# Performance work log

Hardware: AMD Instinct MI355X
Metric: run time of the kernel (lower is better)

The kernel has to match this reference:

```python
import jax, jax.numpy as jnp
import numpy as np

S, B, D, W = 2048, 4, 1024, 256  # seq_len, batch, d_model, local_window_size


def create_local_mask(seq_len, w):
    # Faithful to source: tril(w-1) then tril(-(w-1)) -> keeps j <= i-(w-1)
    m = jnp.ones((seq_len, seq_len), dtype=bool)
    m = jnp.tril(m, w - 1)
    m = jnp.tril(m, -(w - 1))
    return m


def setup_inputs() -> dict:
    key = jax.random.key(0)
    ks = jax.random.split(key, 12)
    w = lambda k: jax.random.normal(k, (D, D), dtype=jnp.float32) * 0.02
    return {
        "query": jax.random.normal(ks[0], (S, B, D), dtype=jnp.float32),
        "key_in": jax.random.normal(ks[1], (S, B, D), dtype=jnp.float32),
        "value": jax.random.normal(ks[2], (S, B, D), dtype=jnp.float32),
        "Wq": w(ks[3]), "bq": jnp.zeros((D,), jnp.float32),
        "Wk": w(ks[4]), "bk": jnp.zeros((D,), jnp.float32),
        "Wv": w(ks[5]), "bv": jnp.zeros((D,), jnp.float32),
        "pos_bias": jax.random.normal(ks[6], (S, S), dtype=jnp.float32) * 0.02,
        "Wo": w(ks[7]), "bo": jnp.zeros((D,), jnp.float32),
        "mask": jnp.ones((S, S, 1), dtype=bool),
    }


def reference(query, key_in, value, Wq, bq, Wk, bk, Wv, bv, pos_bias, Wo, bo, mask):
    # Linear projections (torch Linear: x @ W.T + b)
    q = jnp.einsum('sbd,ed->sbe', query, Wq) + bq
    k = jnp.einsum('sbd,ed->sbe', key_in, Wk) + bk
    v = jnp.einsum('sbd,ed->sbe', value, Wv) + bv

    local_mask = create_local_mask(S, W)
    pb = (pos_bias * local_mask.astype(pos_bias.dtype))[:, :, None]  # [S,S,1]
    pb = jnp.where(mask, pb, -jnp.inf)

    max_key = jnp.max(k, axis=0, keepdims=True)          # [1,B,D]
    max_pb = jnp.max(pb, axis=1, keepdims=True)          # [S,1,1]
    exp_key = jnp.exp(k - max_key)                       # [S,B,D]
    exp_pb = jnp.exp(pb - max_pb)                        # [S,S,B] after broadcast

    num = jnp.einsum('ijb,jbd->ibd', exp_pb, exp_key * v)
    den = jnp.einsum('ijb,jbd->ibd', exp_pb, exp_key)
    y = jax.nn.sigmoid(q) * num / den
    return jnp.einsum('sbd,ed->sbe', y, Wo) + bo
```

## Files before the change

kernel.cpp:

```cpp
#include <hip/hip_runtime.h>
#include <hip/hip_bf16.h>
#include <cstdint>


typedef short short8 __attribute__((ext_vector_type(8)));
typedef float f32x4 __attribute__((ext_vector_type(4)));

#define S_LEN 2048
#define NBD 4096
#define SBD 8388608
#define DD 1048576
#define SS 4194304

#define ASZ 8192
#define BUFSZ 24576
#define AS1 __attribute__((address_space(1)))
#define AS3 __attribute__((address_space(3)))

__device__ __forceinline__ unsigned short f2bf(float f) {
  union { float f; unsigned int u; } x; x.f = f;
  unsigned int u = x.u;
  unsigned int r = u + 0x7fffu + ((u >> 16) & 1u);
  return (unsigned short)(r >> 16);
}
__device__ __forceinline__ float bf2f(unsigned short b) {
  union { unsigned int u; float f; } x; x.u = ((unsigned int)b) << 16;
  return x.f;
}

__global__ void k_cvt3(const float* __restrict__ a, const float* __restrict__ b,
                       const float* __restrict__ c, unsigned short* __restrict__ oa,
                       unsigned short* __restrict__ ob, unsigned short* __restrict__ oc) {
  int i = (blockIdx.x * blockDim.x + threadIdx.x) * 4;
  float4 fa = *(const float4*)(a + i);
  float4 fb = *(const float4*)(b + i);
  float4 fc = *(const float4*)(c + i);
  ushort4 ua, ub, uc;
  ua.x = f2bf(fa.x); ua.y = f2bf(fa.y); ua.z = f2bf(fa.z); ua.w = f2bf(fa.w);
  ub.x = f2bf(fb.x); ub.y = f2bf(fb.y); ub.z = f2bf(fb.z); ub.w = f2bf(fb.w);
  uc.x = f2bf(fc.x); uc.y = f2bf(fc.y); uc.z = f2bf(fc.z); uc.w = f2bf(fc.w);
  *(ushort4*)(oa + i) = ua;
  *(ushort4*)(ob + i) = ub;
  *(ushort4*)(oc + i) = uc;
}

__global__ void k_cvt4w(const float* __restrict__ wq, const float* __restrict__ wk,
                        const float* __restrict__ wv, const float* __restrict__ wo,
                        unsigned short* __restrict__ wcat, unsigned short* __restrict__ wob) {
  int i = (blockIdx.x * blockDim.x + threadIdx.x) * 4;
  float4 fq = *(const float4*)(wq + i);
  float4 fk = *(const float4*)(wk + i);
  float4 fv = *(const float4*)(wv + i);
  float4 fo = *(const float4*)(wo + i);
  ushort4 u;
  u.x = f2bf(fq.x); u.y = f2bf(fq.y); u.z = f2bf(fq.z); u.w = f2bf(fq.w);
  *(ushort4*)(wcat + i) = u;
  u.x = f2bf(fk.x); u.y = f2bf(fk.y); u.z = f2bf(fk.z); u.w = f2bf(fk.w);
  *(ushort4*)(wcat + DD + i) = u;
  u.x = f2bf(fv.x); u.y = f2bf(fv.y); u.z = f2bf(fv.z); u.w = f2bf(fv.w);
  *(ushort4*)(wcat + 2 * DD + i) = u;
  u.x = f2bf(fo.x); u.y = f2bf(fo.y); u.z = f2bf(fo.z); u.w = f2bf(fo.w);
  *(ushort4*)(wob + i) = u;
}

__global__ void k_build_c(const float* __restrict__ pb, unsigned short* __restrict__ C) {
  int idx = blockIdx.x * blockDim.x + threadIdx.x;
  int i = idx >> 11;
  int j = idx & 2047;
  float v = (i >= j + 255) ? expm1f(pb[idx]) : 0.0f;
  C[idx] = f2bf(v);
}

__global__ __launch_bounds__(256) void k_eu_transpose(
    const unsigned short* __restrict__ kbf, const unsigned short* __restrict__ vbf,
    unsigned short* __restrict__ Mt, float* __restrict__ totals) {
  __shared__ unsigned short Lu[64][65];
  __shared__ unsigned short Le[64][65];
  const int n0 = blockIdx.x * 64;
  const int j0 = blockIdx.y * 64;
  const int t = threadIdx.x;
  const int c = t & 63;
  const int jq = t >> 6;
  float ptu = 0.f, pte = 0.f;
#pragma unroll 4
  for (int s = 0; s < 16; ++s) {
    int jj = jq + s * 4;
    size_t g = (size_t)(j0 + jj) * NBD + n0 + c;
    float kv = bf2f(kbf[g]);
    float vv = bf2f(vbf[g]);
    float e = __expf(kv);
    float u = e * vv;
    Le[jj][c] = f2bf(e);
    Lu[jj][c] = f2bf(u);
    pte += e; ptu += u;
  }
  atomicAdd(&totals[n0 + c], ptu);
  atomicAdd(&totals[NBD + n0 + c], pte);
  __syncthreads();
  const int jj2 = t & 63;
  const int nq = t >> 6;
#pragma unroll 4
  for (int s = 0; s < 16; ++s) {
    int nn = nq + s * 4;
    int ru = 2 * n0 + 32 * (nn >> 4) + (nn & 15);
    Mt[(size_t)ru * S_LEN + j0 + jj2] = Lu[jj2][nn];
    Mt[(size_t)(ru + 16) * S_LEN + j0 + jj2] = Le[jj2][nn];
  }
}


#define SBAR() do { __builtin_amdgcn_sched_barrier(0); __builtin_amdgcn_s_barrier(); \
                    __builtin_amdgcn_sched_barrier(0); } while (0)
#define VM(n)  do { asm volatile("s_waitcnt vmcnt(" #n ")" ::: "memory"); \
                    __builtin_amdgcn_sched_barrier(0); } while (0)
#define LGK0() do { asm volatile("s_waitcnt lgkmcnt(0)" ::: "memory"); \
                    __builtin_amdgcn_sched_barrier(0); } while (0)

#define STAGE(tile, bidx) do {                                                            \
    const int k0s_ = (tile) * 64;                                                         \
    _Pragma("unroll") for (int q_ = 0; q_ < 2; ++q_) {                                    \
      const int g_ = wave * 2 + q_;                                                       \
      __builtin_amdgcn_global_load_lds(                                                   \
          (const AS1 unsigned int*)(Ag + (size_t)(m0 + g_ * 8 + lr) * LDA + k0s_ + lc),   \
          (AS3 unsigned int*)&lds[(bidx) * BUFSZ + g_ * 512], 16, 0, 0);                  \
    }                                                                                     \
    _Pragma("unroll") for (int q_ = 0; q_ < 4; ++q_) {                                    \
      const int g_ = wave * 4 + q_;                                                       \
      __builtin_amdgcn_global_load_lds(                                                   \
          (const AS1 unsigned int*)(Bg + (size_t)(n0 + g_ * 8 + lr) * LDB + k0s_ + lc),   \
          (AS3 unsigned int*)&lds[(bidx) * BUFSZ + ASZ + g_ * 512], 16, 0, 0);            \
    }                                                                                     \
  } while (0)

#define READF(RA, RB, bidx, ks) do {                                                      \
    const int kof_ = (ks) * 32 + lh8;                                                     \
    _Pragma("unroll") for (int f_ = 0; f_ < 4; ++f_) {                                    \
      const int row_ = wr + f_ * 16 + l15;                                                \
      RA[f_] = *(const short8*)&lds[(bidx) * BUFSZ + row_ * 64 + (kof_ ^ swz)];           \
    }                                                                                     \
    _Pragma("unroll") for (int f_ = 0; f_ < 4; ++f_) {                                    \
      const int row_ = wc + f_ * 16 + l15;                                                \
      RB[f_] = *(const short8*)&lds[(bidx) * BUFSZ + ASZ + row_ * 64 + (kof_ ^ swz)];     \
    }                                                                                     \
  } while (0)

#define MFMA16(RA, RB) do {                                                               \
    __builtin_amdgcn_s_setprio(1);                                                        \
    _Pragma("unroll") for (int i_ = 0; i_ < 4; ++i_)                                      \
    _Pragma("unroll") for (int j_ = 0; j_ < 4; ++j_)                                      \
      acc[i_][j_] = __builtin_amdgcn_mfma_f32_16x16x32_bf16(RA[i_], RB[j_],               \
                                                            acc[i_][j_], 0, 0, 0);       \
    __builtin_amdgcn_s_setprio(0);                                                        \
  } while (0)

template <int MODE>
__global__ __launch_bounds__(512, 2) void k_gemm8(
    const unsigned short* __restrict__ A0, const unsigned short* __restrict__ A1,
    const unsigned short* __restrict__ A2, const unsigned short* __restrict__ Bg,
    const float* __restrict__ x0, const float* __restrict__ x1, const float* __restrict__ x2,
    const unsigned short* __restrict__ sq,
    void* __restrict__ out0, void* __restrict__ out1, void* __restrict__ out2) {
  __shared__ unsigned short lds[3 * BUFSZ];

  const int tid = threadIdx.x;
  const int wave = tid >> 6, lane = tid & 63;
  const int l15 = lane & 15, lh = lane >> 4;
  const int lh8 = lh * 8;
  const int swz = (l15 & 7) * 8;
  const int lr = lane >> 3;
  const int lc = ((lane & 7) ^ lr) * 8;
  const int wr = (wave >> 2) * 64, wc = (wave & 3) * 64;

  const int w = blockIdx.x;
  int mb, nb;
  if (MODE == 0) { const int xcd = w & 7, slot = w >> 3; mb = xcd * 8 + slot / 12; nb = slot % 12; }
  else if (MODE == 1) { mb = 15 - (w >> 5); nb = w & 31; }
  else { const int xcd = w & 7, slot = w >> 3; mb = xcd * 8 + (slot >> 2); nb = slot & 3; }
  const int m0 = mb * 128, n0 = nb * 256;
  const int LDA = (MODE == 1) ? 2048 : 1024;
  const int LDB = (MODE == 1) ? 2048 : 1024;
  const int NT = (MODE == 1) ? (mb > 0 ? 2 * mb - 1 : 0) : 16;
  const int grp = (MODE == 0) ? (nb >> 2) : 0;
  const unsigned short* Ag = (MODE == 0) ? (grp == 0 ? A0 : (grp == 1 ? A1 : A2)) : A0;

  f32x4 acc[4][4];
#pragma unroll
  for (int i = 0; i < 4; ++i)
#pragma unroll
    for (int j = 0; j < 4; ++j)
      acc[i][j] = (f32x4){0.f, 0.f, 0.f, 0.f};

  short8 ra0[4], rb0[4], ra1[4], rb1[4];

  if (NT > 0) {
    STAGE(0, 0);
    if (NT > 1) STAGE(1, 1);
    if (NT > 2) STAGE(2, 2);
    if (NT > 2) VM(12); else if (NT > 1) VM(6); else VM(0);
    SBAR();
    READF(ra0, rb0, 0, 0);
    int cb = 0;
    for (int t = 0; t < NT; ++t) {
      READF(ra1, rb1, cb, 1);
      MFMA16(ra0, rb0);
      if (t < NT - 1) {
        LGK0();
        if (t + 2 <= NT - 1) VM(6); else VM(0);
        SBAR();
        int nbuf = cb + 1; if (nbuf == 3) nbuf = 0;
        READF(ra0, rb0, nbuf, 0);
        if (t + 3 <= NT - 1) STAGE(t + 3, cb);
        cb = nbuf;
        MFMA16(ra1, rb1);
      } else {
        MFMA16(ra1, rb1);
      }
    }
  }

  if (MODE == 0) {
    const float* bias = grp == 0 ? x0 : (grp == 1 ? x1 : x2);
    unsigned short* outp = (unsigned short*)(grp == 0 ? out0 : (grp == 1 ? out1 : out2));
#pragma unroll
    for (int i = 0; i < 4; ++i)
#pragma unroll
      for (int j = 0; j < 4; ++j)
#pragma unroll
        for (int r = 0; r < 4; ++r) {
          const int row = m0 + wr + i * 16 + lh * 4 + r;
          const int col = (n0 + wc + j * 16 + l15) & 1023;
          float v = acc[i][j][r] + bias[col];
          if (grp == 0) v = 1.0f / (1.0f + __expf(-v));
          outp[(size_t)row * 1024 + col] = f2bf(v);
        }
  } else if (MODE == 1) {
    unsigned short* Y = (unsigned short*)out0;
#pragma unroll
    for (int i = 0; i < 4; ++i)
#pragma unroll
      for (int p = 0; p < 2; ++p) {
        const int n = ((n0 + wc) >> 1) + 16 * p + l15;
        const float tu = x0[n];
        const float te = x0[NBD + n];
#pragma unroll
        for (int r = 0; r < 4; ++r) {
          const int row = m0 + wr + i * 16 + lh * 4 + r;
          const size_t idx = (size_t)row * NBD + n;
          const float num = tu + acc[i][2 * p][r];
          const float den = te + acc[i][2 * p + 1][r];
          Y[idx] = f2bf(bf2f(sq[idx]) * num / den);
        }
      }
  } else {
    float* outp = (float*)out0;
#pragma unroll
    for (int i = 0; i < 4; ++i)
#pragma unroll
      for (int j = 0; j < 4; ++j)
#pragma unroll
        for (int r = 0; r < 4; ++r) {
          const int row = m0 + wr + i * 16 + lh * 4 + r;
          const int col = n0 + wc + j * 16 + l15;
          outp[(size_t)row * 1024 + col] = acc[i][j][r] + x0[col];
        }
  }
}

extern "C" void kernel_launch(void* const* d_in, const int* in_sizes, int n_in,
                              void* d_out, int out_size, void* d_ws, size_t ws_size,
                              hipStream_t stream) {
  const float* query   = (const float*)d_in[0];
  const float* key_in  = (const float*)d_in[1];
  const float* value   = (const float*)d_in[2];
  const float* Wq      = (const float*)d_in[3];
  const float* bq      = (const float*)d_in[4];
  const float* Wk      = (const float*)d_in[5];
  const float* bk      = (const float*)d_in[6];
  const float* Wv      = (const float*)d_in[7];
  const float* bv      = (const float*)d_in[8];
  const float* pos_bias= (const float*)d_in[9];
  const float* Wo      = (const float*)d_in[10];
  const float* bo      = (const float*)d_in[11];
  float* out = (float*)d_out;

  char* wp = (char*)d_ws;
  auto alloc = [&](size_t bytes) -> char* {
    char* p = wp;
    wp += (bytes + 255) & ~(size_t)255;
    return p;
  };
  unsigned short* Xq   = (unsigned short*)alloc((size_t)SBD * 2);
  unsigned short* Xk   = (unsigned short*)alloc((size_t)SBD * 2);
  unsigned short* Xv   = (unsigned short*)alloc((size_t)SBD * 2);
  unsigned short* Wcat = (unsigned short*)alloc((size_t)3 * DD * 2);
  unsigned short* Wob  = (unsigned short*)alloc((size_t)DD * 2);
  unsigned short* Cb   = (unsigned short*)alloc((size_t)SS * 2);
  unsigned short* sigq = (unsigned short*)alloc((size_t)SBD * 2);
  unsigned short* kbf  = (unsigned short*)alloc((size_t)SBD * 2);
  unsigned short* vbf  = (unsigned short*)alloc((size_t)SBD * 2);
  unsigned short* Mt   = (unsigned short*)alloc((size_t)8192 * S_LEN * 2);
  float*          tot  = (float*)alloc((size_t)8192 * 4);
  unsigned short* Yb   = (unsigned short*)alloc((size_t)SBD * 2);

  k_cvt3<<<SBD / 4 / 256, 256, 0, stream>>>(query, key_in, value, Xq, Xk, Xv);
  k_cvt4w<<<DD / 4 / 256, 256, 0, stream>>>(Wq, Wk, Wv, Wo, Wcat, Wob);

  k_build_c<<<SS / 256, 256, 0, stream>>>(pos_bias, Cb);

  k_gemm8<0><<<768, 512, 0, stream>>>(Xq, Xk, Xv, Wcat, bq, bk, bv, nullptr,
                                      sigq, kbf, vbf);

  hipMemsetAsync(tot, 0, 8192 * sizeof(float), stream);
  dim3 ge(NBD / 64, S_LEN / 64);
  k_eu_transpose<<<ge, 256, 0, stream>>>(kbf, vbf, Mt, tot);

  k_gemm8<1><<<512, 512, 0, stream>>>(Cb, nullptr, nullptr, Mt, tot, nullptr, nullptr,
                                      sigq, Yb, nullptr, nullptr);

  k_gemm8<2><<<256, 512, 0, stream>>>(Yb, nullptr, nullptr, Wob, bo, nullptr, nullptr,
                                      nullptr, out, nullptr, nullptr);
}
```

Before: 179.6 us.

## Fuse fp32-to-bf16 input conversion into the QKV projection GEMM

Removes the separate conversion kernel for query/key/value and its bf16 staging buffers. A new QKV GEMM kernel loads fp32 activations into registers, converts them to bf16, and writes them to LDS inside the pipelined main loop, while weights still stream through global_load_lds. This cuts a full read-and-write pass over three 32 MB inputs and one kernel launch. In exchange the GEMM reads twice the bytes for A and spends extra VALU work and register pressure on conversion inside the loop.

```diff
diff --git a/kernel.cpp b/kernel.cpp
--- a/kernel.cpp
+++ b/kernel.cpp
@@ -26,22 +26,6 @@
 __device__ __forceinline__ float bf2f(unsigned short b) {
   union { unsigned int u; float f; } x; x.u = ((unsigned int)b) << 16;
   return x.f;
-}
-
-__global__ void k_cvt3(const float* __restrict__ a, const float* __restrict__ b,
-                       const float* __restrict__ c, unsigned short* __restrict__ oa,
-                       unsigned short* __restrict__ ob, unsigned short* __restrict__ oc) {
-  int i = (blockIdx.x * blockDim.x + threadIdx.x) * 4;
-  float4 fa = *(const float4*)(a + i);
-  float4 fb = *(const float4*)(b + i);
-  float4 fc = *(const float4*)(c + i);
-  ushort4 ua, ub, uc;
-  ua.x = f2bf(fa.x); ua.y = f2bf(fa.y); ua.z = f2bf(fa.z); ua.w = f2bf(fa.w);
-  ub.x = f2bf(fb.x); ub.y = f2bf(fb.y); ub.z = f2bf(fb.z); ub.w = f2bf(fb.w);
-  uc.x = f2bf(fc.x); uc.y = f2bf(fc.y); uc.z = f2bf(fc.z); uc.w = f2bf(fc.w);
-  *(ushort4*)(oa + i) = ua;
-  *(ushort4*)(ob + i) = ub;
-  *(ushort4*)(oc + i) = uc;
 }
 
 __global__ void k_cvt4w(const float* __restrict__ wq, const float* __restrict__ wk,
@@ -108,13 +92,154 @@
   }
 }
 
-
 #define SBAR() do { __builtin_amdgcn_sched_barrier(0); __builtin_amdgcn_s_barrier(); \
                     __builtin_amdgcn_sched_barrier(0); } while (0)
 #define VM(n)  do { asm volatile("s_waitcnt vmcnt(" #n ")" ::: "memory"); \
                     __builtin_amdgcn_sched_barrier(0); } while (0)
 #define LGK0() do { asm volatile("s_waitcnt lgkmcnt(0)" ::: "memory"); \
                     __builtin_amdgcn_sched_barrier(0); } while (0)
+
+#define MFMA16(RA, RB) do {                                                               \
+    __builtin_amdgcn_s_setprio(1);                                                        \
+    _Pragma("unroll") for (int i_ = 0; i_ < 4; ++i_)                                      \
+    _Pragma("unroll") for (int j_ = 0; j_ < 4; ++j_)                                      \
+      acc[i_][j_] = __builtin_amdgcn_mfma_f32_16x16x32_bf16(RA[i_], RB[j_],               \
+                                                            acc[i_][j_], 0, 0, 0);       \
+    __builtin_amdgcn_s_setprio(0);                                                        \
+  } while (0)
+
+#define READF(RA, RB, bidx, ks) do {                                                      \
+    const int kof_ = (ks) * 32 + lh8;                                                     \
+    _Pragma("unroll") for (int f_ = 0; f_ < 4; ++f_) {                                    \
+      const int row_ = wr + f_ * 16 + l15;                                                \
+      RA[f_] = *(const short8*)&lds[(bidx) * BUFSZ + row_ * 64 + (kof_ ^ swz)];           \
+    }                                                                                     \
+    _Pragma("unroll") for (int f_ = 0; f_ < 4; ++f_) {                                    \
+      const int row_ = wc + f_ * 16 + l15;                                                \
+      RB[f_] = *(const short8*)&lds[(bidx) * BUFSZ + ASZ + row_ * 64 + (kof_ ^ swz)];     \
+    }                                                                                     \
+  } while (0)
+
+#define ALD(tile) do {                                                                    \
+    const float* p0_ = aP0 + (tile) * 64;                                                 \
+    const float* p1_ = aP1 + (tile) * 64;                                                 \
+    af00 = *(const float4*)p0_;  af01 = *(const float4*)(p0_ + 4);                        \
+    af10 = *(const float4*)p1_;  af11 = *(const float4*)(p1_ + 4);                        \
+  } while (0)
+
+#define ACVT(bidx) do {                                                                   \
+    short8 s0_, s1_;                                                                      \
+    s0_[0] = (short)f2bf(af00.x); s0_[1] = (short)f2bf(af00.y);                           \
+    s0_[2] = (short)f2bf(af00.z); s0_[3] = (short)f2bf(af00.w);                           \
+    s0_[4] = (short)f2bf(af01.x); s0_[5] = (short)f2bf(af01.y);                           \
+    s0_[6] = (short)f2bf(af01.z); s0_[7] = (short)f2bf(af01.w);                           \
+    s1_[0] = (short)f2bf(af10.x); s1_[1] = (short)f2bf(af10.y);                           \
+    s1_[2] = (short)f2bf(af10.z); s1_[3] = (short)f2bf(af10.w);                           \
+    s1_[4] = (short)f2bf(af11.x); s1_[5] = (short)f2bf(af11.y);                           \
+    s1_[6] = (short)f2bf(af11.z); s1_[7] = (short)f2bf(af11.w);                           \
+    *(short8*)&lds[(bidx) * BUFSZ + da0] = s0_;                                           \
+    *(short8*)&lds[(bidx) * BUFSZ + da1] = s1_;                                           \
+  } while (0)
+
+#define BSTG(tile, bidx) do {                                                             \
+    const int k0s_ = (tile) * 64;                                                         \
+    _Pragma("unroll") for (int q_ = 0; q_ < 4; ++q_) {                                    \
+      const int g_ = wave * 4 + q_;                                                       \
+      __builtin_amdgcn_global_load_lds(                                                   \
+          (const AS1 unsigned int*)(Bg + (size_t)(n0 + g_ * 8 + lr) * 1024 + k0s_ + lc),  \
+          (AS3 unsigned int*)&lds[(bidx) * BUFSZ + ASZ + g_ * 512], 16, 0, 0);            \
+    }                                                                                     \
+  } while (0)
+
+__global__ __launch_bounds__(512, 2) void k_qkvf32(
+    const float* __restrict__ A0, const float* __restrict__ A1,
+    const float* __restrict__ A2, const unsigned short* __restrict__ Bg,
+    const float* __restrict__ b0, const float* __restrict__ b1, const float* __restrict__ b2,
+    unsigned short* __restrict__ o0, unsigned short* __restrict__ o1,
+    unsigned short* __restrict__ o2) {
+  __shared__ unsigned short lds[3 * BUFSZ];
+
+  const int tid = threadIdx.x;
+  const int wave = tid >> 6, lane = tid & 63;
+  const int l15 = lane & 15, lh = lane >> 4;
+  const int lh8 = lh * 8;
+  const int swz = (l15 & 7) * 8;
+  const int lr = lane >> 3;
+  const int lq = lane & 7;
+  const int lc = (lq ^ lr) * 8;
+  const int wr = (wave >> 2) * 64, wc = (wave & 3) * 64;
+
+  const int w = blockIdx.x;
+  const int xcd = w & 7, slot = w >> 3;
+  const int mb = xcd * 8 + slot / 12;
+  const int nb = slot % 12;
+  const int m0 = mb * 128, n0 = nb * 256;
+  const int grp = nb >> 2;
+  const float* Af = grp == 0 ? A0 : (grp == 1 ? A1 : A2);
+
+  const float* aP0 = Af + (size_t)(m0 + (wave * 2 + 0) * 8 + lr) * 1024 + lc;
+  const float* aP1 = Af + (size_t)(m0 + (wave * 2 + 1) * 8 + lr) * 1024 + lc;
+  const int da0 = (wave * 2 + 0) * 512 + lane * 8;
+  const int da1 = (wave * 2 + 1) * 512 + lane * 8;
+
+  f32x4 acc[4][4];
+#pragma unroll
+  for (int i = 0; i < 4; ++i)
+#pragma unroll
+    for (int j = 0; j < 4; ++j)
+      acc[i][j] = (f32x4){0.f, 0.f, 0.f, 0.f};
+
+  float4 af00, af01, af10, af11;
+  short8 ra0[4], rb0[4], ra1[4], rb1[4];
+  const int NT = 16;
+
+  ALD(0); VM(0); ACVT(0);
+  ALD(1); BSTG(0, 0);
+  VM(4);  ACVT(1);
+  ALD(2); BSTG(1, 1);
+  VM(4);  ACVT(2);
+  ALD(3); BSTG(2, 2);
+  LGK0();
+  VM(8);
+  SBAR();
+  READF(ra0, rb0, 0, 0);
+  int cb = 0;
+  for (int t = 0; t < NT; ++t) {
+    READF(ra1, rb1, cb, 1);
+    MFMA16(ra0, rb0);
+    if (t < NT - 1) {
+      LGK0();
+      if (t <= NT - 3) VM(4); else VM(0);
+      SBAR();
+      int nbuf = cb + 1; if (nbuf == 3) nbuf = 0;
+      READF(ra0, rb0, nbuf, 0);
+      if (t + 3 <= NT - 1) ACVT(cb);
+      if (t + 4 <= NT - 1) ALD(t + 4);
+      if (t + 3 <= NT - 1) BSTG(t + 3, cb);
+      __builtin_amdgcn_sched_barrier(0);
+      cb = nbuf;
+      MFMA16(ra1, rb1);
+    } else {
+      MFMA16(ra1, rb1);
+    }
+  }
+
+  const float* bias = grp == 0 ? b0 : (grp == 1 ? b1 : b2);
+  unsigned short* outp = grp == 0 ? o0 : (grp == 1 ? o1 : o2);
+#pragma unroll
+  for (int i = 0; i < 4; ++i)
+#pragma unroll
+    for (int j = 0; j < 4; ++j)
+#pragma unroll
+      for (int r = 0; r < 4; ++r) {
+        const int row = m0 + wr + i * 16 + lh * 4 + r;
+        const int col = (n0 + wc + j * 16 + l15) & 1023;
+        float v = acc[i][j][r] + bias[col];
+        if (grp == 0) v = 1.0f / (1.0f + __expf(-v));
+        outp[(size_t)row * 1024 + col] = f2bf(v);
+      }
+}
+
 
 #define STAGE(tile, bidx) do {                                                            \
     const int k0s_ = (tile) * 64;                                                         \
@@ -132,34 +257,11 @@
     }                                                                                     \
   } while (0)
 
-#define READF(RA, RB, bidx, ks) do {                                                      \
-    const int kof_ = (ks) * 32 + lh8;                                                     \
-    _Pragma("unroll") for (int f_ = 0; f_ < 4; ++f_) {                                    \
-      const int row_ = wr + f_ * 16 + l15;                                                \
-      RA[f_] = *(const short8*)&lds[(bidx) * BUFSZ + row_ * 64 + (kof_ ^ swz)];           \
-    }                                                                                     \
-    _Pragma("unroll") for (int f_ = 0; f_ < 4; ++f_) {                                    \
-      const int row_ = wc + f_ * 16 + l15;                                                \
-      RB[f_] = *(const short8*)&lds[(bidx) * BUFSZ + ASZ + row_ * 64 + (kof_ ^ swz)];     \
-    }                                                                                     \
-  } while (0)
-
-#define MFMA16(RA, RB) do {                                                               \
-    __builtin_amdgcn_s_setprio(1);                                                        \
-    _Pragma("unroll") for (int i_ = 0; i_ < 4; ++i_)                                      \
-    _Pragma("unroll") for (int j_ = 0; j_ < 4; ++j_)                                      \
-      acc[i_][j_] = __builtin_amdgcn_mfma_f32_16x16x32_bf16(RA[i_], RB[j_],               \
-                                                            acc[i_][j_], 0, 0, 0);       \
-    __builtin_amdgcn_s_setprio(0);                                                        \
-  } while (0)
-
 template <int MODE>
 __global__ __launch_bounds__(512, 2) void k_gemm8(
-    const unsigned short* __restrict__ A0, const unsigned short* __restrict__ A1,
-    const unsigned short* __restrict__ A2, const unsigned short* __restrict__ Bg,
-    const float* __restrict__ x0, const float* __restrict__ x1, const float* __restrict__ x2,
-    const unsigned short* __restrict__ sq,
-    void* __restrict__ out0, void* __restrict__ out1, void* __restrict__ out2) {
+    const unsigned short* __restrict__ A0, const unsigned short* __restrict__ Bg,
+    const float* __restrict__ x0, const unsigned short* __restrict__ sq,
+    void* __restrict__ out0) {
   __shared__ unsigned short lds[3 * BUFSZ];
 
   const int tid = threadIdx.x;
@@ -173,15 +275,13 @@
 
   const int w = blockIdx.x;
   int mb, nb;
-  if (MODE == 0) { const int xcd = w & 7, slot = w >> 3; mb = xcd * 8 + slot / 12; nb = slot % 12; }
-  else if (MODE == 1) { mb = 15 - (w >> 5); nb = w & 31; }
+  if (MODE == 1) { mb = 15 - (w >> 5); nb = w & 31; }
   else { const int xcd = w & 7, slot = w >> 3; mb = xcd * 8 + (slot >> 2); nb = slot & 3; }
   const int m0 = mb * 128, n0 = nb * 256;
   const int LDA = (MODE == 1) ? 2048 : 1024;
   const int LDB = (MODE == 1) ? 2048 : 1024;
   const int NT = (MODE == 1) ? (mb > 0 ? 2 * mb - 1 : 0) : 16;
-  const int grp = (MODE == 0) ? (nb >> 2) : 0;
-  const unsigned short* Ag = (MODE == 0) ? (grp == 0 ? A0 : (grp == 1 ? A1 : A2)) : A0;
+  const unsigned short* Ag = A0;
 
   f32x4 acc[4][4];
 #pragma unroll
@@ -218,22 +318,7 @@
     }
   }
 
-  if (MODE == 0) {
-    const float* bias = grp == 0 ? x0 : (grp == 1 ? x1 : x2);
-    unsigned short* outp = (unsigned short*)(grp == 0 ? out0 : (grp == 1 ? out1 : out2));
-#pragma unroll
-    for (int i = 0; i < 4; ++i)
-#pragma unroll
-      for (int j = 0; j < 4; ++j)
-#pragma unroll
-        for (int r = 0; r < 4; ++r) {
-          const int row = m0 + wr + i * 16 + lh * 4 + r;
-          const int col = (n0 + wc + j * 16 + l15) & 1023;
-          float v = acc[i][j][r] + bias[col];
-          if (grp == 0) v = 1.0f / (1.0f + __expf(-v));
-          outp[(size_t)row * 1024 + col] = f2bf(v);
-        }
-  } else if (MODE == 1) {
+  if (MODE == 1) {
     unsigned short* Y = (unsigned short*)out0;
 #pragma unroll
     for (int i = 0; i < 4; ++i)
@@ -289,9 +374,6 @@
     wp += (bytes + 255) & ~(size_t)255;
     return p;
   };
-  unsigned short* Xq   = (unsigned short*)alloc((size_t)SBD * 2);
-  unsigned short* Xk   = (unsigned short*)alloc((size_t)SBD * 2);
-  unsigned short* Xv   = (unsigned short*)alloc((size_t)SBD * 2);
   unsigned short* Wcat = (unsigned short*)alloc((size_t)3 * DD * 2);
   unsigned short* Wob  = (unsigned short*)alloc((size_t)DD * 2);
   unsigned short* Cb   = (unsigned short*)alloc((size_t)SS * 2);
@@ -302,21 +384,18 @@
   float*          tot  = (float*)alloc((size_t)8192 * 4);
   unsigned short* Yb   = (unsigned short*)alloc((size_t)SBD * 2);
 
-  k_cvt3<<<SBD / 4 / 256, 256, 0, stream>>>(query, key_in, value, Xq, Xk, Xv);
   k_cvt4w<<<DD / 4 / 256, 256, 0, stream>>>(Wq, Wk, Wv, Wo, Wcat, Wob);
 
   k_build_c<<<SS / 256, 256, 0, stream>>>(pos_bias, Cb);
 
-  k_gemm8<0><<<768, 512, 0, stream>>>(Xq, Xk, Xv, Wcat, bq, bk, bv, nullptr,
-                                      sigq, kbf, vbf);
+  k_qkvf32<<<768, 512, 0, stream>>>(query, key_in, value, Wcat, bq, bk, bv,
+                                    sigq, kbf, vbf);
 
   hipMemsetAsync(tot, 0, 8192 * sizeof(float), stream);
   dim3 ge(NBD / 64, S_LEN / 64);
   k_eu_transpose<<<ge, 256, 0, stream>>>(kbf, vbf, Mt, tot);
 
-  k_gemm8<1><<<512, 512, 0, stream>>>(Cb, nullptr, nullptr, Mt, tot, nullptr, nullptr,
-                                      sigq, Yb, nullptr, nullptr);
-
-  k_gemm8<2><<<256, 512, 0, stream>>>(Yb, nullptr, nullptr, Wob, bo, nullptr, nullptr,
-                                      nullptr, out, nullptr, nullptr);
-}
+  k_gemm8<1><<<512, 512, 0, stream>>>(Cb, Mt, tot, sigq, Yb);
+
+  k_gemm8<2><<<256, 512, 0, stream>>>(Yb, Wob, bo, nullptr, out);
+}
```

Result: no change. 179.8 us (+0.1%).

## Replace QKV projection GEMM with 256x256-tile kernel using 4-stage pipeline

Applied to the files above, without the earlier changes.

Adds a dedicated QKV projection kernel that computes 256x256 output tiles per block (8x4 MFMA fragments per wave) with a K-step of 32 and a 4-buffer global_load_lds pipeline. It replaces the 128x256-tile generic MODE 0 path. The larger tile is meant to raise arithmetic intensity and cut redundant A/B loads, and the deeper prefetch is meant to hide memory latency. In exchange it uses more registers and LDS, which drops occupancy to one block per CU, and the grid shrinks to 384 blocks.

```diff
diff --git a/kernel.cpp b/kernel.cpp
--- a/kernel.cpp
+++ b/kernel.cpp
@@ -108,13 +108,123 @@
   }
 }
 
-
 #define SBAR() do { __builtin_amdgcn_sched_barrier(0); __builtin_amdgcn_s_barrier(); \
                     __builtin_amdgcn_sched_barrier(0); } while (0)
 #define VM(n)  do { asm volatile("s_waitcnt vmcnt(" #n ")" ::: "memory"); \
                     __builtin_amdgcn_sched_barrier(0); } while (0)
 #define LGK0() do { asm volatile("s_waitcnt lgkmcnt(0)" ::: "memory"); \
                     __builtin_amdgcn_sched_barrier(0); } while (0)
+
+
+#define QSTAGE(tile, BP) do {                                                             \
+    const int t32_ = (tile) * 32;                                                         \
+    _Pragma("unroll") for (int q_ = 0; q_ < 2; ++q_) {                                    \
+      __builtin_amdgcn_global_load_lds(                                                   \
+          (const AS1 unsigned int*)(sA + q_ * 16 * 1024 + t32_),                          \
+          (AS3 unsigned int*)&lds[(BP) * 16384 + (wave * 2 + q_) * 512], 16, 0, 0);       \
+    }                                                                                     \
+    _Pragma("unroll") for (int q_ = 0; q_ < 2; ++q_) {                                    \
+      __builtin_amdgcn_global_load_lds(                                                   \
+          (const AS1 unsigned int*)(sB + q_ * 16 * 1024 + t32_),                          \
+          (AS3 unsigned int*)&lds[(BP) * 16384 + 8192 + (wave * 2 + q_) * 512], 16, 0, 0);\
+    }                                                                                     \
+  } while (0)
+
+#define QREAD(RA, RB, BP) do {                                                            \
+    _Pragma("unroll") for (int f_ = 0; f_ < 8; ++f_)                                      \
+      RA[f_] = *(const short8*)&lds[(BP) * 16384 + rdA + f_ * 512];                       \
+    _Pragma("unroll") for (int f_ = 0; f_ < 4; ++f_)                                      \
+      RB[f_] = *(const short8*)&lds[(BP) * 16384 + rdB + f_ * 512];                       \
+  } while (0)
+
+#define QMFMA(RA, RB) do {                                                                \
+    __builtin_amdgcn_s_setprio(1);                                                        \
+    _Pragma("unroll") for (int i_ = 0; i_ < 8; ++i_)                                      \
+    _Pragma("unroll") for (int j_ = 0; j_ < 4; ++j_)                                      \
+      acc[i_][j_] = __builtin_amdgcn_mfma_f32_16x16x32_bf16(RA[i_], RB[j_],               \
+                                                            acc[i_][j_], 0, 0, 0);       \
+    __builtin_amdgcn_s_setprio(0);                                                        \
+  } while (0)
+
+#define QITER(T, BP, BPN, RAc, RBc, RAn, RBn) do {                                        \
+    QREAD(RAn, RBn, BPN);                                                                 \
+    QMFMA(RAc, RBc);                                                                      \
+    LGK0(); VM(4); SBAR();                                                                \
+    QSTAGE((T) + 4, BP);                                                                  \
+  } while (0)
+
+__global__ __launch_bounds__(512, 1) void k_qkv256(
+    const unsigned short* __restrict__ A0, const unsigned short* __restrict__ A1,
+    const unsigned short* __restrict__ A2, const unsigned short* __restrict__ Bg,
+    const float* __restrict__ b0, const float* __restrict__ b1, const float* __restrict__ b2,
+    unsigned short* __restrict__ o0, unsigned short* __restrict__ o1,
+    unsigned short* __restrict__ o2) {
+  __shared__ unsigned short lds[4 * 16384];
+
+  const int tid = threadIdx.x;
+  const int wave = tid >> 6, lane = tid & 63;
+  const int l15 = lane & 15, lh = lane >> 4;
+  const int wr = (wave >> 2) * 128, wc = (wave & 3) * 64;
+
+  const int w = blockIdx.x;
+  const int xcd = w & 7, slot = w >> 3;
+  const int mb = xcd * 4 + slot / 12;
+  const int nb = slot % 12;
+  const int m0 = mb * 256, n0 = nb * 256;
+  const int grp = nb >> 2;
+  const unsigned short* Ag = grp == 0 ? A0 : (grp == 1 ? A1 : A2);
+
+  const int swz8 = (lh ^ (l15 & 3)) * 8;
+  const int rdA = (wr + l15) * 32 + swz8;
+  const int rdB = 8192 + (wc + l15) * 32 + swz8;
+
+  const int lr16 = lane >> 2;
+  const int csw = ((lane & 3) ^ (lr16 & 3)) * 8;
+  const unsigned short* sA = Ag + (size_t)(m0 + wave * 32 + lr16) * 1024 + csw;
+  const unsigned short* sB = Bg + (size_t)(n0 + wave * 32 + lr16) * 1024 + csw;
+
+  f32x4 acc[8][4];
+#pragma unroll
+  for (int i = 0; i < 8; ++i)
+#pragma unroll
+    for (int j = 0; j < 4; ++j)
+      acc[i][j] = (f32x4){0.f, 0.f, 0.f, 0.f};
+
+  short8 ra0[8], rb0[4], ra1[8], rb1[4];
+
+  QSTAGE(0, 0); QSTAGE(1, 1); QSTAGE(2, 2); QSTAGE(3, 3);
+  VM(8);
+  SBAR();
+  QREAD(ra0, rb0, 0);
+
+#pragma unroll 1
+  for (int tb = 0; tb < 28; tb += 4) {
+    QITER(tb + 0, 0, 1, ra0, rb0, ra1, rb1);
+    QITER(tb + 1, 1, 2, ra1, rb1, ra0, rb0);
+    QITER(tb + 2, 2, 3, ra0, rb0, ra1, rb1);
+    QITER(tb + 3, 3, 0, ra1, rb1, ra0, rb0);
+  }
+  QREAD(ra1, rb1, 1); QMFMA(ra0, rb0); LGK0(); VM(4); SBAR();
+  QREAD(ra0, rb0, 2); QMFMA(ra1, rb1); LGK0(); VM(0); SBAR();
+  QREAD(ra1, rb1, 3); QMFMA(ra0, rb0); LGK0();
+  QMFMA(ra1, rb1);
+
+  const float* bias = grp == 0 ? b0 : (grp == 1 ? b1 : b2);
+  unsigned short* outp = grp == 0 ? o0 : (grp == 1 ? o1 : o2);
+#pragma unroll
+  for (int i = 0; i < 8; ++i)
+#pragma unroll
+    for (int j = 0; j < 4; ++j)
+#pragma unroll
+      for (int r = 0; r < 4; ++r) {
+        const int row = m0 + wr + i * 16 + lh * 4 + r;
+        const int col = (n0 + wc + j * 16 + l15) & 1023;
+        float v = acc[i][j][r] + bias[col];
+        if (grp == 0) v = 1.0f / (1.0f + __expf(-v));
+        outp[(size_t)row * 1024 + col] = f2bf(v);
+      }
+}
+
 
 #define STAGE(tile, bidx) do {                                                            \
     const int k0s_ = (tile) * 64;                                                         \
@@ -155,11 +265,9 @@
 
 template <int MODE>
 __global__ __launch_bounds__(512, 2) void k_gemm8(
-    const unsigned short* __restrict__ A0, const unsigned short* __restrict__ A1,
-    const unsigned short* __restrict__ A2, const unsigned short* __restrict__ Bg,
-    const float* __restrict__ x0, const float* __restrict__ x1, const float* __restrict__ x2,
-    const unsigned short* __restrict__ sq,
-    void* __restrict__ out0, void* __restrict__ out1, void* __restrict__ out2) {
+    const unsigned short* __restrict__ A0, const unsigned short* __restrict__ Bg,
+    const float* __restrict__ x0, const unsigned short* __restrict__ sq,
+    void* __restrict__ out0) {
   __shared__ unsigned short lds[3 * BUFSZ];
 
   const int tid = threadIdx.x;
@@ -173,15 +281,13 @@
 
   const int w = blockIdx.x;
   int mb, nb;
-  if (MODE == 0) { const int xcd = w & 7, slot = w >> 3; mb = xcd * 8 + slot / 12; nb = slot % 12; }
-  else if (MODE == 1) { mb = 15 - (w >> 5); nb = w & 31; }
+  if (MODE == 1) { mb = 15 - (w >> 5); nb = w & 31; }
   else { const int xcd = w & 7, slot = w >> 3; mb = xcd * 8 + (slot >> 2); nb = slot & 3; }
   const int m0 = mb * 128, n0 = nb * 256;
   const int LDA = (MODE == 1) ? 2048 : 1024;
   const int LDB = (MODE == 1) ? 2048 : 1024;
   const int NT = (MODE == 1) ? (mb > 0 ? 2 * mb - 1 : 0) : 16;
-  const int grp = (MODE == 0) ? (nb >> 2) : 0;
-  const unsigned short* Ag = (MODE == 0) ? (grp == 0 ? A0 : (grp == 1 ? A1 : A2)) : A0;
+  const unsigned short* Ag = A0;
 
   f32x4 acc[4][4];
 #pragma unroll
@@ -218,22 +324,7 @@
     }
   }
 
-  if (MODE == 0) {
-    const float* bias = grp == 0 ? x0 : (grp == 1 ? x1 : x2);
-    unsigned short* outp = (unsigned short*)(grp == 0 ? out0 : (grp == 1 ? out1 : out2));
-#pragma unroll
-    for (int i = 0; i < 4; ++i)
-#pragma unroll
-      for (int j = 0; j < 4; ++j)
-#pragma unroll
-        for (int r = 0; r < 4; ++r) {
-          const int row = m0 + wr + i * 16 + lh * 4 + r;
-          const int col = (n0 + wc + j * 16 + l15) & 1023;
-          float v = acc[i][j][r] + bias[col];
-          if (grp == 0) v = 1.0f / (1.0f + __expf(-v));
-          outp[(size_t)row * 1024 + col] = f2bf(v);
-        }
-  } else if (MODE == 1) {
+  if (MODE == 1) {
     unsigned short* Y = (unsigned short*)out0;
 #pragma unroll
     for (int i = 0; i < 4; ++i)
@@ -307,16 +398,13 @@
 
   k_build_c<<<SS / 256, 256, 0, stream>>>(pos_bias, Cb);
 
-  k_gemm8<0><<<768, 512, 0, stream>>>(Xq, Xk, Xv, Wcat, bq, bk, bv, nullptr,
-                                      sigq, kbf, vbf);
+  k_qkv256<<<384, 512, 0, stream>>>(Xq, Xk, Xv, Wcat, bq, bk, bv, sigq, kbf, vbf);
 
   hipMemsetAsync(tot, 0, 8192 * sizeof(float), stream);
   dim3 ge(NBD / 64, S_LEN / 64);
   k_eu_transpose<<<ge, 256, 0, stream>>>(kbf, vbf, Mt, tot);
 
-  k_gemm8<1><<<512, 512, 0, stream>>>(Cb, nullptr, nullptr, Mt, tot, nullptr, nullptr,
-                                      sigq, Yb, nullptr, nullptr);
-
-  k_gemm8<2><<<256, 512, 0, stream>>>(Yb, nullptr, nullptr, Wob, bo, nullptr, nullptr,
-                                      nullptr, out, nullptr, nullptr);
-}
+  k_gemm8<1><<<512, 512, 0, stream>>>(Cb, Mt, tot, sigq, Yb);
+
+  k_gemm8<2><<<256, 512, 0, stream>>>(Yb, Wob, bo, nullptr, out);
+}
```

After: 225.5 us. 1.26x slower.
